# Performance work log

Measured on AMD Instinct MI355X. Metric: run time of the kernel, lower is better.

## Reference

```python
import jax, jax.numpy as jnp
import numpy as np

N_NODES = 50000
N_EDGES = 800000
IN_DIM = 256
HID = 64
LAT = 64
HEADS = 4
NUM_GRAPHS = 64
NEG_SLOPE = 0.2


def _gat_layer(h_in, src, dst, W, a_s, a_d, b, heads, concat):
    N = h_in.shape[0]
    F_ = W.shape[1] // heads
    h = (h_in @ W).reshape(N, heads, F_)              # [N,H,F]
    al_s = jnp.sum(h * a_s, axis=-1)                  # [N,H]
    al_d = jnp.sum(h * a_d, axis=-1)                  # [N,H]
    e = jax.nn.leaky_relu(al_s[src] + al_d[dst], NEG_SLOPE)  # [E,H]
    # scatter-softmax over edges grouped by destination node
    m = jax.ops.segment_max(e, dst, num_segments=N)
    e = jnp.exp(e - m[dst])
    s = jax.ops.segment_sum(e, dst, num_segments=N)
    alpha = e / (s[dst] + 1e-16)                      # [E,H]
    out = jax.ops.segment_sum(h[src] * alpha[:, :, None], dst, num_segments=N)
    out = out.reshape(N, heads * F_) if concat else out.mean(axis=1)
    return out + b


def setup_inputs() -> dict:
    key = jax.random.key(0)
    ks = jax.random.split(key, 20)
    g = lambda k, shp, sc: jax.random.normal(k, shp, jnp.float32) * sc
    inp = {}
    inp['x'] = g(ks[0], (N_NODES, IN_DIM), 1.0)
    inp['edge_index'] = jax.random.randint(ks[1], (2, N_EDGES), 0, N_NODES, jnp.int32)
    inp['batch'] = jnp.sort(jax.random.randint(ks[2], (N_NODES,), 0, NUM_GRAPHS, jnp.int32))
    # layer 0: IN_DIM -> HID, 4 heads, concat
    inp['W1'] = g(ks[3], (IN_DIM, HEADS * HID), 0.05)
    inp['a1s'] = g(ks[4], (HEADS, HID), 0.05)
    inp['a1d'] = g(ks[5], (HEADS, HID), 0.05)
    inp['b1'] = jnp.zeros((HEADS * HID,), jnp.float32)
    # layer 1: 4*HID -> HID, 4 heads, concat
    inp['W2'] = g(ks[6], (HEADS * HID, HEADS * HID), 0.05)
    inp['a2s'] = g(ks[7], (HEADS, HID), 0.05)
    inp['a2d'] = g(ks[8], (HEADS, HID), 0.05)
    inp['b2'] = jnp.zeros((HEADS * HID,), jnp.float32)
    # layer 2: 4*HID -> LAT, 1 head, mean
    inp['W3'] = g(ks[9], (HEADS * HID, LAT), 0.05)
    inp['a3s'] = g(ks[10], (1, LAT), 0.05)
    inp['a3d'] = g(ks[11], (1, LAT), 0.05)
    inp['b3'] = jnp.zeros((LAT,), jnp.float32)
    # VAE head
    inp['Wmu'] = g(ks[12], (LAT, LAT), 0.1)
    inp['bmu'] = jnp.zeros((LAT,), jnp.float32)
    inp['Wlv'] = g(ks[13], (LAT, LAT), 0.1)
    inp['blv'] = jnp.zeros((LAT,), jnp.float32)
    return inp


def reference(x, edge_index, batch, W1, a1s, a1d, b1, W2, a2s, a2d, b2,
              W3, a3s, a3d, b3, Wmu, bmu, Wlv, blv):
    N = x.shape[0]
    loop = jnp.arange(N, dtype=edge_index.dtype)
    src = jnp.concatenate([edge_index[0], loop])   # add self-loops (PyG default)
    dst = jnp.concatenate([edge_index[1], loop])
    h = _gat_layer(x, src, dst, W1, a1s, a1d, b1, HEADS, True)
    h = jax.nn.elu(h)
    h = _gat_layer(h, src, dst, W2, a2s, a2d, b2, HEADS, True)
    h = jax.nn.elu(h)
    h = _gat_layer(h, src, dst, W3, a3s, a3d, b3, 1, False)
    # global mean pool per graph
    sums = jax.ops.segment_sum(h, batch, num_segments=NUM_GRAPHS)
    cnts = jax.ops.segment_sum(jnp.ones((N,), h.dtype), batch, num_segments=NUM_GRAPHS)
    pooled = sums / jnp.maximum(cnts, 1.0)[:, None]  # [G, LAT]
    mu = pooled @ Wmu + bmu
    logvar = pooled @ Wlv + blv
    std = jnp.exp(0.5 * logvar)
    eps = jax.random.normal(jax.random.key(42), std.shape, std.dtype)
    z = mu + eps * std
    return (mu, logvar, z)
```

## Files before the change

kernel.cpp:

```cpp
#include <hip/hip_runtime.h>
#include <hip/hip_bf16.h>
#include <cstdint>
#include <math.h>


#define N_NODES 50000
#define N_EDGES 800000
#define NEG_SLOPE 0.2f

typedef __hip_bfloat16 bf16;
typedef short short8 __attribute__((ext_vector_type(8)));
typedef float floatx4 __attribute__((ext_vector_type(4)));
typedef float floatx2 __attribute__((ext_vector_type(2)));

__device__ __forceinline__ float bf2f(bf16 v){ return __bfloat162float(v); }
__device__ __forceinline__ float bflo(unsigned u){ union{unsigned u; float f;} c; c.u = u<<16; return c.f; }
__device__ __forceinline__ float bfhi(unsigned u){ union{unsigned u; float f;} c; c.u = u & 0xFFFF0000u; return c.f; }
__device__ __forceinline__ float leaky(float v){ return v>0.f ? v : NEG_SLOPE*v; }
__device__ __forceinline__ unsigned short f2bu(float f){
  union{ bf16 b; unsigned short u; } c; c.b = __float2bfloat16(f); return c.u;
}
__device__ __forceinline__ unsigned char f2fp8(float v){
  int p = __builtin_amdgcn_cvt_pk_fp8_f32(v, v, 0, false);
  return (unsigned char)(p & 0xff);
}
__device__ __forceinline__ void acc_fp8x4(float* acc, unsigned wrd, float wgt){
  floatx2 lo = __builtin_amdgcn_cvt_pk_f32_fp8((int)wrd, false);
  floatx2 hi = __builtin_amdgcn_cvt_pk_f32_fp8((int)wrd, true);
  acc[0] = fmaf(lo[0], wgt, acc[0]);
  acc[1] = fmaf(lo[1], wgt, acc[1]);
  acc[2] = fmaf(hi[0], wgt, acc[2]);
  acc[3] = fmaf(hi[1], wgt, acc[3]);
}

__device__ __forceinline__ void tf_round(unsigned& x0, unsigned& x1, int r){
  x0 += x1; x1 = (x1<<r)|(x1>>(32-r)); x1 ^= x0;
}
__device__ __forceinline__ void threefry2x32(unsigned k0, unsigned k1, unsigned& x0, unsigned& x1){
  unsigned ks2 = k0 ^ k1 ^ 0x1BD11BDAu;
  x0 += k0; x1 += k1;
  tf_round(x0,x1,13); tf_round(x0,x1,15); tf_round(x0,x1,26); tf_round(x0,x1,6);
  x0 += k1; x1 += ks2 + 1u;
  tf_round(x0,x1,17); tf_round(x0,x1,29); tf_round(x0,x1,16); tf_round(x0,x1,24);
  x0 += ks2; x1 += k0 + 2u;
  tf_round(x0,x1,13); tf_round(x0,x1,15); tf_round(x0,x1,26); tf_round(x0,x1,6);
  x0 += k0; x1 += k1 + 3u;
  tf_round(x0,x1,17); tf_round(x0,x1,29); tf_round(x0,x1,16); tf_round(x0,x1,24);
  x0 += k1; x1 += ks2 + 4u;
  tf_round(x0,x1,13); tf_round(x0,x1,15); tf_round(x0,x1,26); tf_round(x0,x1,6);
  x0 += ks2; x1 += k0 + 5u;
}

__device__ __forceinline__ float erfinv_approx(float x){
  float w = -log1pf(-x*x);
  float p;
  if (w < 5.0f){
    w = w - 2.5f;
    p = 2.81022636e-08f;
    p = fmaf(p,w,3.43273939e-07f);
    p = fmaf(p,w,-3.5233877e-06f);
    p = fmaf(p,w,-4.39150654e-06f);
    p = fmaf(p,w,0.00021858087f);
    p = fmaf(p,w,-0.00125372503f);
    p = fmaf(p,w,-0.00417768164f);
    p = fmaf(p,w,0.246640727f);
    p = fmaf(p,w,1.50140941f);
  } else {
    w = sqrtf(w) - 3.0f;
    p = -0.000200214257f;
    p = fmaf(p,w,0.000100950558f);
    p = fmaf(p,w,0.00134934322f);
    p = fmaf(p,w,-0.00367342844f);
    p = fmaf(p,w,0.00573950773f);
    p = fmaf(p,w,-0.0076224613f);
    p = fmaf(p,w,0.00943887047f);
    p = fmaf(p,w,1.00167406f);
    p = fmaf(p,w,2.83297682f);
  }
  return p*x;
}

__global__ __launch_bounds__(256) void wt_all_kernel(
        const float* __restrict__ W1, const float* __restrict__ W2,
        const float* __restrict__ W3, short* __restrict__ Wt1,
        short* __restrict__ Wt2, short* __restrict__ Wt3){
  const float* W; short* Wt; int Nn;
  if (blockIdx.z == 0){ W = W1; Wt = Wt1; Nn = 256; }
  else if (blockIdx.z == 1){ W = W2; Wt = Wt2; Nn = 256; }
  else { W = W3; Wt = Wt3; Nn = 64; }
  const int n0 = blockIdx.x*32, k0 = blockIdx.y*32;
  if (n0 >= Nn) return;
  __shared__ float tile[32][33];
  const int tx = threadIdx.x & 31, ty = threadIdx.x >> 5;
  #pragma unroll
  for (int i=0;i<4;++i)
    tile[ty+8*i][tx] = W[(size_t)(k0+ty+8*i)*Nn + n0 + tx];
  __syncthreads();
  #pragma unroll
  for (int i=0;i<4;++i)
    Wt[(size_t)(n0+ty+8*i)*256 + k0 + tx] = (short)f2bu(tile[tx][ty+8*i]);
}

template<int OUT, bool INBF>
__global__ __launch_bounds__(256) void gemm_mfma_kernel(const void* __restrict__ inp,
        const short* __restrict__ Wt, void* __restrict__ outv,
        const float* __restrict__ a_s, const float* __restrict__ a_d,
        float* __restrict__ als, float* __restrict__ ald, int N){
  constexpr int M_BLK = (OUT==256) ? 64 : 256;
  constexpr int H = (OUT==256) ? 4 : 1;
  __shared__ short As[M_BLK*48];
  __shared__ short Bs[OUT*48];
  const int t = threadIdx.x;
  const int w = t>>6, lane = t&63;
  const int lm = lane&15, g = lane>>4;
  const int m0 = blockIdx.x * M_BLK;
  const int m_off = (OUT==256) ? 0 : w*64;
  const int n0    = (OUT==256) ? w*64 : 0;

  floatx4 acc[4][4] = {};

  for (int kk=0; kk<8; ++kk){
    const int k0 = kk*32;
    __syncthreads();
    for (int a = t; a < M_BLK*4; a += 256){
      int r = a>>2, c = a&3;
      int gr = m0 + r;
      uint4 v = make_uint4(0u,0u,0u,0u);
      if (gr < N){
        if constexpr (INBF){
          v = *(const uint4*)((const bf16*)inp + (size_t)gr*256 + k0 + c*8);
        } else {
          const float* p = (const float*)inp + (size_t)gr*256 + k0 + c*8;
          float4 f0 = *(const float4*)p;
          float4 f1 = *(const float4*)(p+4);
          v.x = (unsigned)f2bu(f0.x) | ((unsigned)f2bu(f0.y)<<16);
          v.y = (unsigned)f2bu(f0.z) | ((unsigned)f2bu(f0.w)<<16);
          v.z = (unsigned)f2bu(f1.x) | ((unsigned)f2bu(f1.y)<<16);
          v.w = (unsigned)f2bu(f1.z) | ((unsigned)f2bu(f1.w)<<16);
        }
      }
      *(uint4*)&As[r*48 + c*8] = v;
    }
    for (int a = t; a < OUT*4; a += 256){
      int r = a>>2, c = a&3;
      uint4 v = *(const uint4*)(Wt + (size_t)r*256 + k0 + c*8);
      *(uint4*)&Bs[r*48 + c*8] = v;
    }
    __syncthreads();
    short8 af[4], bfr[4];
    #pragma unroll
    for (int mt=0;mt<4;++mt)
      af[mt] = *(const short8*)&As[(m_off + mt*16 + lm)*48 + g*8];
    #pragma unroll
    for (int nt=0;nt<4;++nt)
      bfr[nt] = *(const short8*)&Bs[(n0 + nt*16 + lm)*48 + g*8];
    #pragma unroll
    for (int mt=0;mt<4;++mt)
      #pragma unroll
      for (int nt=0;nt<4;++nt)
        acc[mt][nt] = __builtin_amdgcn_mfma_f32_16x16x32_bf16(af[mt], bfr[nt], acc[mt][nt], 0, 0, 0);
  }

  float asv[4], adv[4];
  #pragma unroll
  for (int nt=0;nt<4;++nt){
    asv[nt] = a_s[n0 + nt*16 + lm];
    adv[nt] = a_d[n0 + nt*16 + lm];
  }
  const int head = (OUT==256) ? w : 0;
  #pragma unroll
  for (int mt=0;mt<4;++mt){
    #pragma unroll
    for (int reg=0;reg<4;++reg){
      int gr = m0 + m_off + mt*16 + g*4 + reg;
      bool valid = gr < N;
      float ps = 0.f, pd = 0.f;
      #pragma unroll
      for (int nt=0;nt<4;++nt){
        float v = acc[mt][nt][reg];
        if (valid){
          if constexpr (OUT==256){
            ((unsigned char*)outv)[(size_t)gr*256 + n0 + nt*16 + lm] = f2fp8(v);
          } else {
            ((bf16*)outv)[(size_t)gr*OUT + n0 + nt*16 + lm] = __float2bfloat16(v);
          }
        }
        ps = fmaf(v, asv[nt], ps);
        pd = fmaf(v, adv[nt], pd);
      }
      #pragma unroll
      for (int o=1;o<16;o<<=1){ ps += __shfl_xor(ps,o); pd += __shfl_xor(pd,o); }
      if (lm==0 && valid){
        als[gr*H + head] = ps;
        ald[gr*H + head] = pd;
      }
    }
  }
}

__global__ void count_kernel(const int* __restrict__ ei, int* __restrict__ deg, int E){
  int e = blockIdx.x*blockDim.x+threadIdx.x; if (e<E) atomicAdd(&deg[ei[E+e]], 1);
}
__global__ void assign_kernel(const int* __restrict__ deg, int* __restrict__ off,
        int* __restrict__ cursor, int* __restrict__ total, int N){
  int i = blockIdx.x*blockDim.x+threadIdx.x;
  if (i<N){
    int d = deg[i] + 1;
    int start = atomicAdd(total, d);
    off[i] = start; cursor[i] = start;
  }
}
__global__ void fill_kernel(const int* __restrict__ ei, int* __restrict__ cursor,
        int* __restrict__ csr_src, int E, int N){
  int e = blockIdx.x*blockDim.x+threadIdx.x;
  if (e >= E+N) return;
  int s_ = (e < E) ? ei[e]   : e-E;
  int d_ = (e < E) ? ei[E+e] : e-E;
  int p = atomicAdd(&cursor[d_], 1);
  csr_src[p] = s_;
}

template<bool ELU>
__global__ __launch_bounds__(64) void aggregate4_kernel(const unsigned char* __restrict__ h8,
        const float* __restrict__ als, const float* __restrict__ ald,
        const int* __restrict__ off, const int* __restrict__ deg,
        const int* __restrict__ csr_src,
        const float* __restrict__ bias, bf16* __restrict__ out){
  __shared__ int   s_src[64];
  __shared__ float s_w[64][4];
  const int n = blockIdx.x, lane = threadIdx.x;
  const int r = lane>>4;
  const int f = lane&15;
  const int head = f>>2;
  const int p0 = off[n], cnt = deg[n]+1;
  const float4 aldn4 = *(const float4*)(ald + n*4);
  float ssum = 0.f;
  float acc[16] = {};
  for (int c=0; c<cnt; c+=64){
    int e = c + lane;
    int src = n; float4 w4 = make_float4(0.f,0.f,0.f,0.f);
    if (e < cnt){
      src = csr_src[p0+e];
      float4 av = *(const float4*)(als + src*4);
      w4.x = expf(leaky(av.x + aldn4.x));
      w4.y = expf(leaky(av.y + aldn4.y));
      w4.z = expf(leaky(av.z + aldn4.z));
      w4.w = expf(leaky(av.w + aldn4.w));
    }
    s_src[lane] = src;
    *(float4*)&s_w[lane][0] = w4;
    int ce = min(64, cnt - c);
    int cp = (ce+7)&~7;
    for (int i=0;i<cp;i+=8){
      int src0 = s_src[i+r], src1 = s_src[i+4+r];
      float w0 = s_w[i+r][head], w1 = s_w[i+4+r][head];
      uint4 h0 = *(const uint4*)(h8 + (size_t)src0*256 + f*16);
      uint4 h1 = *(const uint4*)(h8 + (size_t)src1*256 + f*16);
      ssum += w0 + w1;
      acc_fp8x4(acc+0,  h0.x, w0); acc_fp8x4(acc+4,  h0.y, w0);
      acc_fp8x4(acc+8,  h0.z, w0); acc_fp8x4(acc+12, h0.w, w0);
      acc_fp8x4(acc+0,  h1.x, w1); acc_fp8x4(acc+4,  h1.y, w1);
      acc_fp8x4(acc+8,  h1.z, w1); acc_fp8x4(acc+12, h1.w, w1);
    }
  }
  #pragma unroll
  for (int j=0;j<16;++j){
    acc[j] += __shfl_xor(acc[j], 16);
    acc[j] += __shfl_xor(acc[j], 32);
  }
  ssum += __shfl_xor(ssum, 16);
  ssum += __shfl_xor(ssum, 32);
  if (r==0){
    float inv = 1.f/(ssum + 1e-16f);
    #pragma unroll
    for (int half=0; half<2; ++half){
      float4 b0 = *(const float4*)(bias + f*16 + half*8);
      float4 b1 = *(const float4*)(bias + f*16 + half*8 + 4);
      float rv[8];
      rv[0]=acc[half*8+0]*inv+b0.x; rv[1]=acc[half*8+1]*inv+b0.y;
      rv[2]=acc[half*8+2]*inv+b0.z; rv[3]=acc[half*8+3]*inv+b0.w;
      rv[4]=acc[half*8+4]*inv+b1.x; rv[5]=acc[half*8+5]*inv+b1.y;
      rv[6]=acc[half*8+6]*inv+b1.z; rv[7]=acc[half*8+7]*inv+b1.w;
      union{ bf16 b[8]; uint4 u; } pk;
      #pragma unroll
      for (int j=0;j<8;++j){
        float v = rv[j];
        if (ELU) v = (v>0.f)?v:expm1f(v);
        pk.b[j] = __float2bfloat16(v);
      }
      *(uint4*)(out + (size_t)n*256 + f*16 + half*8) = pk.u;
    }
  }
}

__global__ __launch_bounds__(64) void aggregate1_kernel(const bf16* __restrict__ h,
        const float* __restrict__ als, const float* __restrict__ ald,
        const int* __restrict__ off, const int* __restrict__ deg,
        const int* __restrict__ csr_src,
        const float* __restrict__ bias, bf16* __restrict__ out){
  __shared__ int   s_src[64];
  __shared__ float s_w[64];
  const int n = blockIdx.x, lane = threadIdx.x;
  const int r = lane>>4;
  const int f = lane&15;
  const int p0 = off[n], cnt = deg[n]+1;
  const float aldn = ald[n];
  float ssum = 0.f;
  float acc[4] = {};
  for (int c=0; c<cnt; c+=64){
    int e = c + lane;
    int src = n; float wv = 0.f;
    if (e < cnt){
      src = csr_src[p0+e];
      wv = expf(leaky(als[src] + aldn));
    }
    s_src[lane] = src; s_w[lane] = wv;
    int ce = min(64, cnt - c);
    int cp = (ce+7)&~7;
    for (int i=0;i<cp;i+=8){
      int src0 = s_src[i+r], src1 = s_src[i+4+r];
      float w0 = s_w[i+r],   w1 = s_w[i+4+r];
      uint2 h0 = *(const uint2*)(h + (size_t)src0*64 + f*4);
      uint2 h1 = *(const uint2*)(h + (size_t)src1*64 + f*4);
      ssum += w0 + w1;
      acc[0]=fmaf(bflo(h0.x),w0,acc[0]); acc[1]=fmaf(bfhi(h0.x),w0,acc[1]);
      acc[2]=fmaf(bflo(h0.y),w0,acc[2]); acc[3]=fmaf(bfhi(h0.y),w0,acc[3]);
      acc[0]=fmaf(bflo(h1.x),w1,acc[0]); acc[1]=fmaf(bfhi(h1.x),w1,acc[1]);
      acc[2]=fmaf(bflo(h1.y),w1,acc[2]); acc[3]=fmaf(bfhi(h1.y),w1,acc[3]);
    }
  }
  #pragma unroll
  for (int j=0;j<4;++j){
    acc[j] += __shfl_xor(acc[j], 16);
    acc[j] += __shfl_xor(acc[j], 32);
  }
  ssum += __shfl_xor(ssum, 16);
  ssum += __shfl_xor(ssum, 32);
  if (r==0){
    float inv = 1.f/(ssum + 1e-16f);
    union{ bf16 b[4]; uint2 u; } pk;
    #pragma unroll
    for (int j=0;j<4;++j) pk.b[j] = __float2bfloat16(acc[j]*inv + bias[f*4+j]);
    *(uint2*)(out + (size_t)n*64 + f*4) = pk.u;
  }
}

__global__ __launch_bounds__(64) void pool_kernel(const bf16* __restrict__ h3,
        const int* __restrict__ batch, float* __restrict__ psum, float* __restrict__ pcnt,
        int N, int chunk){
  int n0 = blockIdx.x*chunk;
  if (n0 >= N) return;
  int n1 = min(N, n0+chunk);
  int t = threadIdx.x;
  int gcur = batch[n0];
  float acc = 0.f, cnt = 0.f;
  for (int n=n0; n<n1; ++n){
    int g = batch[n];
    if (g != gcur){
      atomicAdd(&psum[gcur*64+t], acc);
      if (t==0) atomicAdd(&pcnt[gcur], cnt);
      acc = 0.f; cnt = 0.f; gcur = g;
    }
    acc += bf2f(h3[(size_t)n*64+t]);
    cnt += 1.f;
  }
  atomicAdd(&psum[gcur*64+t], acc);
  if (t==0) atomicAdd(&pcnt[gcur], cnt);
}

__global__ __launch_bounds__(64) void head_kernel(const float* __restrict__ psum,
        const float* __restrict__ pcnt,
        const float* __restrict__ Wmu, const float* __restrict__ bmu,
        const float* __restrict__ Wlv, const float* __restrict__ blv,
        float* __restrict__ out){
  int g = blockIdx.x, t = threadIdx.x;
  __shared__ float p[64];
  float cnt = fmaxf(pcnt[g], 1.0f);
  p[t] = psum[g*64+t] / cnt;
  __syncthreads();
  float mu = bmu[t], lv = blv[t];
  for (int k=0;k<64;++k){
    float pk = p[k];
    mu = fmaf(pk, Wmu[(size_t)k*64+t], mu);
    lv = fmaf(pk, Wlv[(size_t)k*64+t], lv);
  }
  int i = g*64 + t;
  unsigned x0 = 0u, x1 = (unsigned)i;
  threefry2x32(0u, 42u, x0, x1);
  unsigned bits = x0 ^ x1;
  float f = __uint_as_float((bits>>9) | 0x3F800000u) - 1.0f;
  const float lo = __uint_as_float(0xBF7FFFFFu);
  float u = fmaxf(lo, f*2.0f + lo);
  float eps = 1.41421356f * erfinv_approx(u);
  float z = mu + eps * expf(0.5f*lv);
  out[i]        = mu;
  out[4096 + i] = lv;
  out[8192 + i] = z;
}

extern "C" void kernel_launch(void* const* d_in, const int* in_sizes, int n_in,
                              void* d_out, int out_size, void* d_ws, size_t ws_size,
                              hipStream_t stream){
  const float* x    = (const float*)d_in[0];
  const int*   ei   = (const int*)d_in[1];
  const int*   batch= (const int*)d_in[2];
  const float* W1   = (const float*)d_in[3];
  const float* a1s  = (const float*)d_in[4];
  const float* a1d  = (const float*)d_in[5];
  const float* b1   = (const float*)d_in[6];
  const float* W2   = (const float*)d_in[7];
  const float* a2s  = (const float*)d_in[8];
  const float* a2d  = (const float*)d_in[9];
  const float* b2   = (const float*)d_in[10];
  const float* W3   = (const float*)d_in[11];
  const float* a3s  = (const float*)d_in[12];
  const float* a3d  = (const float*)d_in[13];
  const float* b3   = (const float*)d_in[14];
  const float* Wmu  = (const float*)d_in[15];
  const float* bmu  = (const float*)d_in[16];
  const float* Wlv  = (const float*)d_in[17];
  const float* blv  = (const float*)d_in[18];
  float* out = (float*)d_out;

  const int N = N_NODES, E = N_EDGES;
  const int ET = E + N;

  char* ws = (char*)d_ws;
  size_t o = 0;
  auto alloc = [&](size_t bytes)->void*{
    void* p = ws + o; o += (bytes + 255) & ~(size_t)255; return p;
  };
  bf16*  hA      = (bf16*) alloc((size_t)N*256*2);
  unsigned char* hB8 = (unsigned char*)alloc((size_t)N*256);
  bf16*  h3      = (bf16*) alloc((size_t)N*64*2);
  float* als     = (float*)alloc((size_t)N*4*4);
  float* ald     = (float*)alloc((size_t)N*4*4);
  int*   deg     = (int*)  alloc((size_t)(N+1)*4);
  int*   total   = deg + N;
  int*   off     = (int*)  alloc((size_t)N*4);
  int*   cursor  = (int*)  alloc((size_t)N*4);
  int*   csr_src = (int*)  alloc((size_t)ET*4);
  short* Wt1     = (short*)alloc(256*256*2);
  short* Wt2     = (short*)alloc(256*256*2);
  short* Wt3     = (short*)alloc(64*256*2);
  float* psum    = (float*)alloc(64*64*4 + 64*4);
  float* pcnt    = psum + 64*64;
  (void)ws_size; (void)n_in; (void)in_sizes; (void)out_size;

  const int TB = 256;
  const int egrid = (ET + TB - 1)/TB;

  wt_all_kernel<<<dim3(8,8,3), 256, 0, stream>>>(W1, W2, W3, Wt1, Wt2, Wt3);

  hipMemsetAsync(deg, 0, (size_t)(N+1)*4, stream);
  count_kernel<<<(E+TB-1)/TB, TB, 0, stream>>>(ei, deg, E);
  assign_kernel<<<(N+TB-1)/TB, TB, 0, stream>>>(deg, off, cursor, total, N);
  fill_kernel<<<egrid, TB, 0, stream>>>(ei, cursor, csr_src, E, N);

  gemm_mfma_kernel<256,false><<<(N+63)/64, 256, 0, stream>>>(x, Wt1, hB8, a1s, a1d, als, ald, N);
  aggregate4_kernel<true><<<N, 64, 0, stream>>>(hB8, als, ald, off, deg, csr_src, b1, hA);

  gemm_mfma_kernel<256,true><<<(N+63)/64, 256, 0, stream>>>(hA, Wt2, hB8, a2s, a2d, als, ald, N);
  aggregate4_kernel<true><<<N, 64, 0, stream>>>(hB8, als, ald, off, deg, csr_src, b2, hA);

  gemm_mfma_kernel<64,true><<<(N+255)/256, 256, 0, stream>>>(hA, Wt3, h3, a3s, a3d, als, ald, N);
  aggregate1_kernel<<<N, 64, 0, stream>>>(h3, als, ald, off, deg, csr_src, b3, hA);

  hipMemsetAsync(psum, 0, 64*64*4 + 64*4, stream);
  const int PBLK = 512;
  const int chunk = (N + PBLK - 1)/PBLK;
  pool_kernel<<<PBLK, 64, 0, stream>>>(hA, batch, psum, pcnt, N, chunk);
  head_kernel<<<64, 64, 0, stream>>>(psum, pcnt, Wmu, bmu, Wlv, blv, out);
}
```

Measured before the change: 460.6 us.

## Unroll aggregation gathers, use packed FMA and fast exp, batch CSR build atomics

The aggregation loops now handle 16 edges per iteration instead of 8, so four independent neighbor rows are loaded at once and more memory latency can overlap. The fp8 accumulation switches to packed float2 multiply-adds, and expf is replaced by the faster, less precise __expf. The count and fill kernels each process four edges per thread, issuing their loads and atomics in batches. In exchange the kernels use more registers and pad more when degrees are small, and __expf slightly reduces accuracy.

```diff
diff --git a/kernel.cpp b/kernel.cpp
--- a/kernel.cpp
+++ b/kernel.cpp
@@ -24,13 +24,16 @@
   int p = __builtin_amdgcn_cvt_pk_fp8_f32(v, v, 0, false);
   return (unsigned char)(p & 0xff);
 }
-__device__ __forceinline__ void acc_fp8x4(float* acc, unsigned wrd, float wgt){
-  floatx2 lo = __builtin_amdgcn_cvt_pk_f32_fp8((int)wrd, false);
-  floatx2 hi = __builtin_amdgcn_cvt_pk_f32_fp8((int)wrd, true);
-  acc[0] = fmaf(lo[0], wgt, acc[0]);
-  acc[1] = fmaf(lo[1], wgt, acc[1]);
-  acc[2] = fmaf(hi[0], wgt, acc[2]);
-  acc[3] = fmaf(hi[1], wgt, acc[3]);
+__device__ __forceinline__ void acc8_pk(floatx2* a, uint4 hv, float w){
+  floatx2 w2; w2[0]=w; w2[1]=w;
+  a[0] += __builtin_amdgcn_cvt_pk_f32_fp8((int)hv.x, false) * w2;
+  a[1] += __builtin_amdgcn_cvt_pk_f32_fp8((int)hv.x, true ) * w2;
+  a[2] += __builtin_amdgcn_cvt_pk_f32_fp8((int)hv.y, false) * w2;
+  a[3] += __builtin_amdgcn_cvt_pk_f32_fp8((int)hv.y, true ) * w2;
+  a[4] += __builtin_amdgcn_cvt_pk_f32_fp8((int)hv.z, false) * w2;
+  a[5] += __builtin_amdgcn_cvt_pk_f32_fp8((int)hv.z, true ) * w2;
+  a[6] += __builtin_amdgcn_cvt_pk_f32_fp8((int)hv.w, false) * w2;
+  a[7] += __builtin_amdgcn_cvt_pk_f32_fp8((int)hv.w, true ) * w2;
 }
 
 __device__ __forceinline__ void tf_round(unsigned& x0, unsigned& x1, int r){
@@ -198,8 +201,18 @@
   }
 }
 
-__global__ void count_kernel(const int* __restrict__ ei, int* __restrict__ deg, int E){
-  int e = blockIdx.x*blockDim.x+threadIdx.x; if (e<E) atomicAdd(&deg[ei[E+e]], 1);
+__global__ void count_kernel(const int* __restrict__ ei, int* __restrict__ deg,
+        int E, int stride){
+  int tid = blockIdx.x*blockDim.x+threadIdx.x;
+  int d[4]; bool v[4];
+  #pragma unroll
+  for (int j=0;j<4;++j){
+    int e = tid + j*stride;
+    v[j] = e < E;
+    d[j] = v[j] ? ei[E+e] : 0;
+  }
+  #pragma unroll
+  for (int j=0;j<4;++j) if (v[j]) atomicAdd(&deg[d[j]], 1);
 }
 __global__ void assign_kernel(const int* __restrict__ deg, int* __restrict__ off,
         int* __restrict__ cursor, int* __restrict__ total, int N){
@@ -211,13 +224,24 @@
   }
 }
 __global__ void fill_kernel(const int* __restrict__ ei, int* __restrict__ cursor,
-        int* __restrict__ csr_src, int E, int N){
-  int e = blockIdx.x*blockDim.x+threadIdx.x;
-  if (e >= E+N) return;
-  int s_ = (e < E) ? ei[e]   : e-E;
-  int d_ = (e < E) ? ei[E+e] : e-E;
-  int p = atomicAdd(&cursor[d_], 1);
-  csr_src[p] = s_;
+        int* __restrict__ csr_src, int E, int N, int stride){
+  int tid = blockIdx.x*blockDim.x+threadIdx.x;
+  const int ET = E + N;
+  int s[4], d[4]; bool v[4];
+  #pragma unroll
+  for (int j=0;j<4;++j){
+    int e = tid + j*stride;
+    v[j] = e < ET;
+    if (v[j]){
+      s[j] = (e < E) ? ei[e]   : e-E;
+      d[j] = (e < E) ? ei[E+e] : e-E;
+    }
+  }
+  int p[4];
+  #pragma unroll
+  for (int j=0;j<4;++j) if (v[j]) p[j] = atomicAdd(&cursor[d[j]], 1);
+  #pragma unroll
+  for (int j=0;j<4;++j) if (v[j]) csr_src[p[j]] = s[j];
 }
 
 template<bool ELU>
@@ -235,34 +259,41 @@
   const int p0 = off[n], cnt = deg[n]+1;
   const float4 aldn4 = *(const float4*)(ald + n*4);
   float ssum = 0.f;
-  float acc[16] = {};
+  floatx2 acc2[8] = {};
   for (int c=0; c<cnt; c+=64){
     int e = c + lane;
     int src = n; float4 w4 = make_float4(0.f,0.f,0.f,0.f);
     if (e < cnt){
       src = csr_src[p0+e];
       float4 av = *(const float4*)(als + src*4);
-      w4.x = expf(leaky(av.x + aldn4.x));
-      w4.y = expf(leaky(av.y + aldn4.y));
-      w4.z = expf(leaky(av.z + aldn4.z));
-      w4.w = expf(leaky(av.w + aldn4.w));
+      w4.x = __expf(leaky(av.x + aldn4.x));
+      w4.y = __expf(leaky(av.y + aldn4.y));
+      w4.z = __expf(leaky(av.z + aldn4.z));
+      w4.w = __expf(leaky(av.w + aldn4.w));
     }
     s_src[lane] = src;
     *(float4*)&s_w[lane][0] = w4;
     int ce = min(64, cnt - c);
-    int cp = (ce+7)&~7;
-    for (int i=0;i<cp;i+=8){
-      int src0 = s_src[i+r], src1 = s_src[i+4+r];
-      float w0 = s_w[i+r][head], w1 = s_w[i+4+r][head];
+    int cp = (ce+15)&~15;
+    for (int i=0;i<cp;i+=16){
+      int src0 = s_src[i+r],   src1 = s_src[i+4+r];
+      int src2 = s_src[i+8+r], src3 = s_src[i+12+r];
+      float w0 = s_w[i+r][head],   w1 = s_w[i+4+r][head];
+      float w2 = s_w[i+8+r][head], w3 = s_w[i+12+r][head];
       uint4 h0 = *(const uint4*)(h8 + (size_t)src0*256 + f*16);
       uint4 h1 = *(const uint4*)(h8 + (size_t)src1*256 + f*16);
-      ssum += w0 + w1;
-      acc_fp8x4(acc+0,  h0.x, w0); acc_fp8x4(acc+4,  h0.y, w0);
-      acc_fp8x4(acc+8,  h0.z, w0); acc_fp8x4(acc+12, h0.w, w0);
-      acc_fp8x4(acc+0,  h1.x, w1); acc_fp8x4(acc+4,  h1.y, w1);
-      acc_fp8x4(acc+8,  h1.z, w1); acc_fp8x4(acc+12, h1.w, w1);
-    }
-  }
+      uint4 h2 = *(const uint4*)(h8 + (size_t)src2*256 + f*16);
+      uint4 h3 = *(const uint4*)(h8 + (size_t)src3*256 + f*16);
+      ssum += (w0 + w1) + (w2 + w3);
+      acc8_pk(acc2, h0, w0);
+      acc8_pk(acc2, h1, w1);
+      acc8_pk(acc2, h2, w2);
+      acc8_pk(acc2, h3, w3);
+    }
+  }
+  float acc[16];
+  #pragma unroll
+  for (int j=0;j<8;++j){ acc[2*j]=acc2[j][0]; acc[2*j+1]=acc2[j][1]; }
   #pragma unroll
   for (int j=0;j<16;++j){
     acc[j] += __shfl_xor(acc[j], 16);
@@ -312,21 +343,29 @@
     int src = n; float wv = 0.f;
     if (e < cnt){
       src = csr_src[p0+e];
-      wv = expf(leaky(als[src] + aldn));
+      wv = __expf(leaky(als[src] + aldn));
     }
     s_src[lane] = src; s_w[lane] = wv;
     int ce = min(64, cnt - c);
-    int cp = (ce+7)&~7;
-    for (int i=0;i<cp;i+=8){
-      int src0 = s_src[i+r], src1 = s_src[i+4+r];
+    int cp = (ce+15)&~15;
+    for (int i=0;i<cp;i+=16){
+      int src0 = s_src[i+r],   src1 = s_src[i+4+r];
+      int src2 = s_src[i+8+r], src3 = s_src[i+12+r];
       float w0 = s_w[i+r],   w1 = s_w[i+4+r];
+      float w2 = s_w[i+8+r], w3 = s_w[i+12+r];
       uint2 h0 = *(const uint2*)(h + (size_t)src0*64 + f*4);
       uint2 h1 = *(const uint2*)(h + (size_t)src1*64 + f*4);
-      ssum += w0 + w1;
+      uint2 h2 = *(const uint2*)(h + (size_t)src2*64 + f*4);
+      uint2 h3 = *(const uint2*)(h + (size_t)src3*64 + f*4);
+      ssum += (w0 + w1) + (w2 + w3);
       acc[0]=fmaf(bflo(h0.x),w0,acc[0]); acc[1]=fmaf(bfhi(h0.x),w0,acc[1]);
       acc[2]=fmaf(bflo(h0.y),w0,acc[2]); acc[3]=fmaf(bfhi(h0.y),w0,acc[3]);
       acc[0]=fmaf(bflo(h1.x),w1,acc[0]); acc[1]=fmaf(bfhi(h1.x),w1,acc[1]);
       acc[2]=fmaf(bflo(h1.y),w1,acc[2]); acc[3]=fmaf(bfhi(h1.y),w1,acc[3]);
+      acc[0]=fmaf(bflo(h2.x),w2,acc[0]); acc[1]=fmaf(bfhi(h2.x),w2,acc[1]);
+      acc[2]=fmaf(bflo(h2.y),w2,acc[2]); acc[3]=fmaf(bfhi(h2.y),w2,acc[3]);
+      acc[0]=fmaf(bflo(h3.x),w3,acc[0]); acc[1]=fmaf(bfhi(h3.x),w3,acc[1]);
+      acc[2]=fmaf(bflo(h3.y),w3,acc[2]); acc[3]=fmaf(bfhi(h3.y),w3,acc[3]);
     }
   }
   #pragma unroll
@@ -448,14 +487,21 @@
   (void)ws_size; (void)n_in; (void)in_sizes; (void)out_size;
 
   const int TB = 256;
-  const int egrid = (ET + TB - 1)/TB;
 
   wt_all_kernel<<<dim3(8,8,3), 256, 0, stream>>>(W1, W2, W3, Wt1, Wt2, Wt3);
 
   hipMemsetAsync(deg, 0, (size_t)(N+1)*4, stream);
-  count_kernel<<<(E+TB-1)/TB, TB, 0, stream>>>(ei, deg, E);
+  {
+    int cthreads = (E + 3)/4;
+    int cgrid = (cthreads + TB - 1)/TB;
+    count_kernel<<<cgrid, TB, 0, stream>>>(ei, deg, E, cgrid*TB);
+  }
   assign_kernel<<<(N+TB-1)/TB, TB, 0, stream>>>(deg, off, cursor, total, N);
-  fill_kernel<<<egrid, TB, 0, stream>>>(ei, cursor, csr_src, E, N);
+  {
+    int fthreads = (ET + 3)/4;
+    int fgrid = (fthreads + TB - 1)/TB;
+    fill_kernel<<<fgrid, TB, 0, stream>>>(ei, cursor, csr_src, E, N, fgrid*TB);
+  }
 
   gemm_mfma_kernel<256,false><<<(N+63)/64, 256, 0, stream>>>(x, Wt1, hB8, a1s, a1d, als, ald, N);
   aggregate4_kernel<true><<<N, 64, 0, stream>>>(hB8, als, ald, off, deg, csr_src, b1, hA);
```

Measured after the change: 478.9 us. 4.0% more time.
